# Performance work log

Measured on AMD Instinct MI355X. Metric: run time of the kernel, lower is better.

Reference implementation:

```python
import jax, jax.numpy as jnp
import numpy as np
import math

B, T, TE, D, H = 1, 2048, 1024, 1024, 16
HD = D // H
INF = 1e9  # infinity_proxy from the original module
INIT_SCALE = 0.02


def sinusoid_pos_emb(timesteps, dim):
    # Transformer-XL sinusoids for relative positions [timesteps-1 .. 0].
    inv_freq = 1.0 / (10000.0 ** (np.arange(0, dim, 2) / dim))
    pos_seq = np.arange(timesteps - 1, -1, -1.0)
    inp = np.einsum('i,j->ij', pos_seq, inv_freq)
    return np.concatenate([np.sin(inp), np.cos(inp)], axis=-1).astype(np.float32)


def relative_shift(x):
    # x: [b, h, t, T] -> TXL left-pad / reshape / slice shift trick.
    b, h, t1, t2 = x.shape
    x = jnp.pad(x, ((0, 0), (0, 0), (0, 0), (1, 0)))
    x = x.reshape(b, h, t2 + 1, t1)[:, :, 1:, :]
    return x.reshape(b, h, t1, t2)


def setup_inputs() -> dict:
    key = jax.random.key(0)
    ks = jax.random.split(key, 12)
    s = INIT_SCALE
    x = jax.random.normal(ks[0], (B, T, D), jnp.float32)
    extra = jax.random.normal(ks[1], (B, TE, D), jnp.float32)
    # causal mask over the in-sequence keys; full visibility on the extra memory
    mask = jnp.broadcast_to(jnp.tril(jnp.ones((T, T), jnp.float32))[None, None], (B, 1, T, T))
    extra_mask = jnp.ones((B, 1, T, TE), jnp.float32)
    Wq = jax.random.normal(ks[2], (D, D), jnp.float32) * s
    Wk = jax.random.normal(ks[3], (D, D), jnp.float32) * s
    Wv = jax.random.normal(ks[4], (D, D), jnp.float32) * s
    Wek = jax.random.normal(ks[5], (D, D), jnp.float32) * s
    Wev = jax.random.normal(ks[6], (D, D), jnp.float32) * s
    Wr = jax.random.normal(ks[7], (D, D), jnp.float32) * s
    Wo = jax.random.normal(ks[8], (D, D), jnp.float32) * s
    r_w_bias = jax.random.normal(ks[9], (H, HD), jnp.float32) * s
    r_r_bias = jax.random.normal(ks[10], (H, HD), jnp.float32) * s
    return dict(x=x, extra=extra, mask=mask, extra_mask=extra_mask,
                Wq=Wq, Wk=Wk, Wv=Wv, Wek=Wek, Wev=Wev, Wr=Wr, Wo=Wo,
                r_w_bias=r_w_bias, r_r_bias=r_r_bias)


def reference(x, extra, mask, extra_mask, Wq, Wk, Wv, Wek, Wev, Wr, Wo, r_w_bias, r_r_bias):
    b, t, d = x.shape
    te = extra.shape[1]
    # conv1d(kernel=1, no bias) == matmul projections; cache_steps=0 so y == x
    q = (x @ Wq).reshape(b, t, H, HD)
    k = (x @ Wk).reshape(b, t, H, HD)
    v = (x @ Wv).reshape(b, t, H, HD)
    # Transformer-XL relative-position attend_fn
    pos = jnp.asarray(sinusoid_pos_emb(t, d))            # [t, D]
    r = (pos @ Wr).reshape(t, H, HD)                      # [t, H, HD]
    content = jnp.einsum('bthd,bThd->bhtT', q + r_w_bias, k)
    rel = relative_shift(jnp.einsum('bthd,Thd->bhtT', q + r_r_bias, r))
    attn = content + rel
    attn = attn * mask - INF * (1.0 - mask)
    # extra keys/values use plain dot-product attention (no rel-pos)
    ek = (extra @ Wek).reshape(b, te, H, HD)
    ev = (extra @ Wev).reshape(b, te, H, HD)
    eattn = jnp.einsum('bthd,bThd->bhtT', q, ek)
    eattn = eattn * extra_mask - INF * (1.0 - extra_mask)
    attn = jnp.concatenate([attn, eattn], axis=-1) * (1.0 / math.sqrt(HD))
    p = jax.nn.softmax(attn, axis=-1)
    vv = jnp.concatenate([v, ev], axis=1)                 # [b, t+te, H, HD]
    out = jnp.einsum('bhtT,bThd->bthd', p, vv).reshape(b, t, d)
    return out @ Wo  # final conv1d, with_final_bias=False
```

## Files before the change

### kernel.cpp

```cpp
#include <hip/hip_runtime.h>
#include <hip/hip_bf16.h>
#include <math.h>

#define T_LEN 2048
#define TE_LEN 1024
#define D_DIM 1024
#define H_NUM 16
#define HD_DIM 64
#define R_PAD 64

typedef unsigned short ushort;
typedef __attribute__((ext_vector_type(8))) short short8;
typedef __attribute__((ext_vector_type(4))) float f32x4;
typedef __attribute__((ext_vector_type(4))) ushort ushort4v;

__device__ __forceinline__ ushort f2b(float f) {
    unsigned u = __builtin_bit_cast(unsigned, f);
    u += 0x7fffu + ((u >> 16) & 1u);
    return (ushort)(u >> 16);
}
__device__ __forceinline__ float b2f(ushort s) {
    unsigned u = ((unsigned)s) << 16;
    return __builtin_bit_cast(float, u);
}

__device__ __forceinline__ void gld16(const ushort* g, ushort* l) {
    __builtin_amdgcn_global_load_lds(
        (const __attribute__((address_space(1))) unsigned int*)g,
        (__attribute__((address_space(3))) unsigned int*)l, 16, 0, 0);
}

union U8 { short8 v; ushort u[8]; };

__global__ void prep_kernel(const float* __restrict__ x, const float* __restrict__ extra,
                            ushort* __restrict__ pos, ushort* __restrict__ xb,
                            ushort* __restrict__ eb) {
    const int q = blockIdx.x * 256 + threadIdx.x;
    const int PQ = 524288;
    const int XQ = 1048576;
    if (q < PQ) {
        int idx = q * 4;
        int i = idx >> 10, j = idx & 1023;
        bool sinreg = (j < 512);
        int jj = sinreg ? j : j - 512;
        float p = (float)(2047 - i);
        ushort4v o;
#pragma unroll
        for (int u = 0; u < 4; u++) {
            float inv = exp2f((float)(jj + u) * -0.025952563241f);
            float fa = p * inv;
            ((ushort*)&o)[u] = f2b(sinreg ? sinf(fa) : cosf(fa));
        }
        *(ushort4v*)&pos[idx] = o;
    } else if (q < XQ) {
        int idx = (q - PQ) * 4;
        float4 v = *(const float4*)&x[idx];
        ushort4v o = {f2b(v.x), f2b(v.y), f2b(v.z), f2b(v.w)};
        *(ushort4v*)&xb[idx] = o;
    } else {
        int idx = (q - XQ) * 4;
        float4 v = *(const float4*)&extra[idx];
        ushort4v o = {f2b(v.x), f2b(v.y), f2b(v.z), f2b(v.w)};
        *(ushort4v*)&eb[idx] = o;
    }
}

__global__ __launch_bounds__(256) void transpose7_kernel(
    const float* __restrict__ W0, const float* __restrict__ W1,
    const float* __restrict__ W2, const float* __restrict__ W3,
    const float* __restrict__ W4, const float* __restrict__ W5,
    const float* __restrict__ W6, ushort* __restrict__ out,
    ushort* __restrict__ Rpad) {
    if (blockIdx.z == 7) {
        int gid = (blockIdx.y * 32 + blockIdx.x) * 256 + threadIdx.x;
        if (gid < (R_PAD * 1024) / 8) {
            short8 z = {0, 0, 0, 0, 0, 0, 0, 0};
            *(short8*)&Rpad[gid * 8] = z;
        }
        return;
    }
    const float* Ws[7] = {W0, W1, W2, W3, W4, W5, W6};
    const float* W = Ws[blockIdx.z];
    ushort* WT = out + (size_t)blockIdx.z * (1024 * 1024);
    __shared__ float tile[32][33];
    int c0 = blockIdx.x * 32, r0 = blockIdx.y * 32;
    int tid = threadIdx.x;
#pragma unroll
    for (int p = 0; p < 4; p++) {
        int idx = tid + p * 256;
        int r = idx >> 5, c = idx & 31;
        tile[r][c] = W[(size_t)(r0 + r) * D_DIM + c0 + c];
    }
    __syncthreads();
#pragma unroll
    for (int p = 0; p < 4; p++) {
        int idx = tid + p * 256;
        int r = idx >> 5, c = idx & 31;
        WT[(size_t)(c0 + r) * D_DIM + r0 + c] = f2b(tile[c][r]);
    }
}

__global__ __launch_bounds__(256) void gemm_mega(
    const ushort* __restrict__ xb, const ushort* __restrict__ posb,
    const ushort* __restrict__ eb, const ushort* __restrict__ WT,
    ushort* __restrict__ Qb, ushort* __restrict__ Kb, ushort* __restrict__ VTb,
    ushort* __restrict__ Rb, ushort* __restrict__ EKb, ushort* __restrict__ EVTb) {
    __shared__ ushort As[128 * 64];
    __shared__ ushort Bs[128 * 64];
    const int tid = threadIdx.x;
    const int lane = tid & 63, w = tid >> 6;
    const int l15 = lane & 15, quad = lane >> 4;
    const int wm = w & 1, wn = w >> 1;
    const size_t M1 = 1024 * 1024;

    int idx = blockIdx.x;
    const ushort *A, *BT;
    ushort* dst;
    int m0, nb0, nc0, ldt = 1024;
    bool transp = false;
    if (idx < 384) {
        m0 = (idx & 15) * 128; nb0 = (idx >> 4) * 128;
        A = xb; BT = WT;
        nc0 = nb0 & 1023;
        int seg = nb0 >> 10;
        if (seg == 0) dst = Qb;
        else if (seg == 1) dst = Kb;
        else { dst = VTb; transp = true; ldt = T_LEN; }
    } else if (idx < 512) {
        int i = idx - 384;
        m0 = (i & 15) * 128; nb0 = (i >> 4) * 128; nc0 = nb0;
        A = posb; BT = WT + 5 * M1; dst = Rb;
    } else {
        int i = idx - 512;
        m0 = (i & 7) * 128; nb0 = (i >> 3) * 128; nc0 = nb0 & 1023;
        A = eb; BT = WT + 3 * M1;
        if (nb0 < 1024) dst = EKb;
        else { dst = EVTb; transp = true; ldt = TE_LEN; }
    }

    f32x4 acc[16];
#pragma unroll
    for (int i = 0; i < 16; i++) acc[i] = (f32x4){0.f, 0.f, 0.f, 0.f};

    for (int k0 = 0; k0 < 1024; k0 += 64) {
        __syncthreads();
#pragma unroll
        for (int i = 0; i < 4; i++) {
            int ci = i * 256 + tid;
            int row = ci >> 3, cs = (ci & 7) ^ (row & 7);
            gld16(A + (size_t)(m0 + row) * 1024 + k0 + cs * 8, &As[(i * 32 + w * 8) * 64]);
            gld16(BT + (size_t)(nb0 + row) * 1024 + k0 + cs * 8, &Bs[(i * 32 + w * 8) * 64]);
        }
        __syncthreads();
#pragma unroll
        for (int kc = 0; kc < 2; kc++) {
            short8 bfr[4];
#pragma unroll
            for (int nf = 0; nf < 4; nf++) {
                const int row = wn * 64 + nf * 16 + l15;
                bfr[nf] = *(const short8*)&Bs[(row * 8 + ((kc * 4 + quad) ^ (row & 7))) * 8];
            }
#pragma unroll
            for (int mf = 0; mf < 4; mf++) {
                const int row = wm * 64 + mf * 16 + l15;
                short8 afr = *(const short8*)&As[(row * 8 + ((kc * 4 + quad) ^ (row & 7))) * 8];
#pragma unroll
                for (int nf = 0; nf < 4; nf++)
                    acc[mf * 4 + nf] = __builtin_amdgcn_mfma_f32_16x16x32_bf16(afr, bfr[nf], acc[mf * 4 + nf], 0, 0, 0);
            }
        }
    }

#pragma unroll
    for (int mf = 0; mf < 4; mf++) {
#pragma unroll
        for (int nf = 0; nf < 4; nf++) {
            f32x4 a = acc[mf * 4 + nf];
            const int mrow = m0 + wm * 64 + mf * 16 + quad * 4;
            const int nc = nc0 + wn * 64 + nf * 16 + l15;
            if (transp) {
                ushort4v v = {f2b(a[0]), f2b(a[1]), f2b(a[2]), f2b(a[3])};
                *(ushort4v*)&dst[(size_t)nc * ldt + mrow] = v;
            } else {
#pragma unroll
                for (int r = 0; r < 4; r++) dst[(size_t)(mrow + r) * 1024 + nc] = f2b(a[r]);
            }
        }
    }
}

__global__ __launch_bounds__(256) void gemm_wo(const ushort* __restrict__ A,
                                               const ushort* __restrict__ BT,
                                               float* __restrict__ out) {
    __shared__ ushort As[128 * 64];
    __shared__ ushort Bs[64 * 64];
    const int tid = threadIdx.x;
    const int lane = tid & 63, w = tid >> 6;
    const int l15 = lane & 15, quad = lane >> 4;
    const int wm = w & 1, wn = w >> 1;
    const int m0 = blockIdx.y * 128, n0 = blockIdx.x * 64;

    f32x4 acc[8];
#pragma unroll
    for (int i = 0; i < 8; i++) acc[i] = (f32x4){0.f, 0.f, 0.f, 0.f};

    for (int k0 = 0; k0 < 1024; k0 += 64) {
        __syncthreads();
#pragma unroll
        for (int i = 0; i < 4; i++) {
            int ci = i * 256 + tid;
            int row = ci >> 3, cs = (ci & 7) ^ (row & 7);
            gld16(A + (size_t)(m0 + row) * 1024 + k0 + cs * 8, &As[(i * 32 + w * 8) * 64]);
        }
#pragma unroll
        for (int i = 0; i < 2; i++) {
            int ci = i * 256 + tid;
            int row = ci >> 3, cs = (ci & 7) ^ (row & 7);
            gld16(BT + (size_t)(n0 + row) * 1024 + k0 + cs * 8, &Bs[(i * 32 + w * 8) * 64]);
        }
        __syncthreads();
#pragma unroll
        for (int kc = 0; kc < 2; kc++) {
            short8 bfr[2];
#pragma unroll
            for (int nf = 0; nf < 2; nf++) {
                const int row = wn * 32 + nf * 16 + l15;
                bfr[nf] = *(const short8*)&Bs[(row * 8 + ((kc * 4 + quad) ^ (row & 7))) * 8];
            }
#pragma unroll
            for (int mf = 0; mf < 4; mf++) {
                const int row = wm * 64 + mf * 16 + l15;
                short8 afr = *(const short8*)&As[(row * 8 + ((kc * 4 + quad) ^ (row & 7))) * 8];
#pragma unroll
                for (int nf = 0; nf < 2; nf++)
                    acc[mf * 2 + nf] = __builtin_amdgcn_mfma_f32_16x16x32_bf16(afr, bfr[nf], acc[mf * 2 + nf], 0, 0, 0);
            }
        }
    }

#pragma unroll
    for (int mf = 0; mf < 4; mf++) {
#pragma unroll
        for (int nf = 0; nf < 2; nf++) {
            f32x4 a = acc[mf * 2 + nf];
            const int mrow = m0 + wm * 64 + mf * 16 + quad * 4;
            const int nc = n0 + wn * 32 + nf * 16 + l15;
#pragma unroll
            for (int r = 0; r < 4; r++) out[(size_t)(mrow + r) * 1024 + nc] = a[r];
        }
    }
}

__global__ __launch_bounds__(256) void attn_kernel(
    const ushort* __restrict__ Qb, const ushort* __restrict__ Kb,
    const ushort* __restrict__ VT, const ushort* __restrict__ Rb,
    const ushort* __restrict__ EKb, const ushort* __restrict__ EVT,
    const float* __restrict__ rwb, const float* __restrict__ rrb,
    float* __restrict__ Of, float* __restrict__ lsum) {
    __shared__ ushort Kst[2][32 * 64];
    __shared__ ushort Vst[2][64 * 32];
    __shared__ ushort Rst[128 * 64];
    __shared__ ushort Plds[4][16 * 40];

    const int tid = threadIdx.x;
    const int lane = tid & 63, wl = tid >> 6;
    const int l15 = lane & 15, quad = lane >> 4;
    const int blk = blockIdx.x;
    const int xcd = blk & 7;
    const int u = blk >> 3;
    const int g = u & 1;
    const int v = u >> 1;
    const int rnd = v >> 5, qslot = v & 31;
    const int h = xcd * 2 + rnd;
    const int qt = rnd ? qslot : 31 - qslot;
    const int t0 = qt * 64, tf = t0 + wl * 16;
    const int hbase = h * HD_DIM;
    const int base0 = 1984 - t0;
    const int ninl = qt + 1;
    const int ntotl = ninl + 16;
    const int tt_s = g * ninl;
    const int baseg = base0 + 32 * tt_s;

    short8 qw[2], qr[2], qp[2];
#pragma unroll
    for (int kh = 0; kh < 2; kh++) {
        int dof = hbase + kh * 32 + quad * 8;
        U8 raw; raw.v = *(const short8*)&Qb[(size_t)(tf + l15) * D_DIM + dof];
        U8 a, b, c;
#pragma unroll
        for (int j = 0; j < 8; j++) {
            float f = b2f(raw.u[j]);
            a.u[j] = f2b((f + rwb[dof + j]) * 0.125f);
            b.u[j] = f2b((f + rrb[dof + j]) * 0.125f);
            c.u[j] = f2b(f * 0.125f);
        }
        qw[kh] = a.v; qr[kh] = b.v; qp[kh] = c.v;
    }

    float lr[4] = {0.f, 0.f, 0.f, 0.f};
    f32x4 O[4];
#pragma unroll
    for (int i = 0; i < 4; i++) O[i] = (f32x4){0.f, 0.f, 0.f, 0.f};
    f32x4 rel_carry = (f32x4){0.f, 0.f, 0.f, 0.f};

    auto stageKV = [&](int i2, int buf) {
        const bool ins = i2 < ninl;
        const int j0 = ins ? (tt_s + i2) * 32 : (g * 16 + (i2 - ninl)) * 32;
        const ushort* ksrc = ins ? Kb : EKb;
        const ushort* vsrc = ins ? VT : EVT;
        const int ldv = ins ? T_LEN : TE_LEN;
        {
            int row = tid >> 3, cs = (tid & 7) ^ (row & 7);
            gld16(ksrc + (size_t)(j0 + row) * 1024 + hbase + cs * 8, &Kst[buf][wl * 512]);
        }
        {
            int row = tid >> 2, cs = (tid & 3) ^ (row & 3);
            gld16(vsrc + (size_t)(hbase + row) * ldv + j0 + cs * 8, &Vst[buf][wl * 512]);
        }
    };
    auto stageR = [&](int slotbase, int rowbase) {
        int k = tid >> 3;
        int s = slotbase + k;
        int cs = (tid & 7) ^ (s & 7);
        gld16(Rb + (size_t)(rowbase + k) * 1024 + hbase + cs * 8,
              &Rst[(slotbase + wl * 8) * 64]);
    };

#pragma unroll
    for (int i = 0; i < 3; i++) {
        int ci = i * 256 + tid;
        int k = ci >> 3, cs = (ci & 7) ^ (k & 7);
        gld16(Rb + (size_t)(baseg + k) * 1024 + hbase + cs * 8, &Rst[(i * 32 + wl * 8) * 64]);
    }
    stageKV(0, 0);

    int srcA[4]; bool lowcA[4];
#pragma unroll
    for (int r = 0; r < 4; r++) {
        const int m = quad * 4 + r;
        const int cb = 15 - m + l15;
        srcA[r] = (lane & 48) | (cb & 15);
        lowcA[r] = (cb < 16);
    }

#pragma unroll 1
    for (int i = 0; i < ntotl; i++) {
        const int b = i & 1;
        __syncthreads();
        if (i + 1 < ntotl) {
            stageKV(i + 1, 1 - b);
            if (i + 1 < ninl) stageR((96 + 32 * i) & 127, baseg + 96 + 32 * i);
        }

        const bool ins = i < ninl;
        const int j0 = (tt_s + i) * 32;

        f32x4 con[2];
#pragma unroll
        for (int c = 0; c < 2; c++) con[c] = (f32x4){0.f, 0.f, 0.f, 0.f};
#pragma unroll
        for (int kh = 0; kh < 2; kh++) {
            const short8* qa = ins ? &qw[kh] : &qp[kh];
#pragma unroll
            for (int nh = 0; nh < 2; nh++) {
                const int row = nh * 16 + l15;
                short8 kf = *(const short8*)&Kst[b][(row * 8 + ((kh * 4 + quad) ^ (row & 7))) * 8];
                con[nh] = __builtin_amdgcn_mfma_f32_16x16x32_bf16(*qa, kf, con[nh], 0, 0, 0);
            }
        }

        if (ins) {
            f32x4 relA, rel1, rel2;
            rel1 = (f32x4){0.f, 0.f, 0.f, 0.f};
            rel2 = (f32x4){0.f, 0.f, 0.f, 0.f};
#pragma unroll
            for (int kh = 0; kh < 2; kh++) {
                const int s1 = (64 - 16 * wl + 32 * i + l15) & 127;
                const int s2 = (80 - 16 * wl + 32 * i + l15) & 127;
                short8 rf1 = *(const short8*)&Rst[(s1 * 8 + ((kh * 4 + quad) ^ (s1 & 7))) * 8];
                short8 rf2 = *(const short8*)&Rst[(s2 * 8 + ((kh * 4 + quad) ^ (s2 & 7))) * 8];
                rel1 = __builtin_amdgcn_mfma_f32_16x16x32_bf16(qr[kh], rf1, rel1, 0, 0, 0);
                rel2 = __builtin_amdgcn_mfma_f32_16x16x32_bf16(qr[kh], rf2, rel2, 0, 0, 0);
            }
            if (i == 0) {
                relA = (f32x4){0.f, 0.f, 0.f, 0.f};
#pragma unroll
                for (int kh = 0; kh < 2; kh++) {
                    const int s0 = (48 - 16 * wl + l15) & 127;
                    short8 rf0 = *(const short8*)&Rst[(s0 * 8 + ((kh * 4 + quad) ^ (s0 & 7))) * 8];
                    relA = __builtin_amdgcn_mfma_f32_16x16x32_bf16(qr[kh], rf0, relA, 0, 0, 0);
                }
            } else {
                relA = rel_carry;
            }
            rel_carry = rel2;

            const bool needmask = (j0 + 31 > tf);
#pragma unroll
            for (int r = 0; r < 4; r++) {
                const int m = quad * 4 + r;
                float b0 = __shfl(relA[r], srcA[r]);
                float b1 = __shfl(rel1[r], srcA[r]);
                float b2 = __shfl(rel2[r], srcA[r]);
                float rv0 = lowcA[r] ? b0 : b1, rv1 = lowcA[r] ? b1 : b2;
                float p0 = __expf(con[0][r] + rv0);
                float p1 = __expf(con[1][r] + rv1);
                if (needmask) {
                    const int t = tf + m;
                    if (j0 + l15 > t)      p0 = 0.f;
                    if (j0 + 16 + l15 > t) p1 = 0.f;
                }
                lr[r] += p0 + p1;
                Plds[wl][m * 40 + l15]      = f2b(p0);
                Plds[wl][m * 40 + 16 + l15] = f2b(p1);
            }
        } else {
#pragma unroll
            for (int r = 0; r < 4; r++) {
                const int m = quad * 4 + r;
                float p0 = __expf(con[0][r]);
                float p1 = __expf(con[1][r]);
                lr[r] += p0 + p1;
                Plds[wl][m * 40 + l15]      = f2b(p0);
                Plds[wl][m * 40 + 16 + l15] = f2b(p1);
            }
        }

        short8 pa = *(const short8*)&Plds[wl][l15 * 40 + quad * 8];
#pragma unroll
        for (int df = 0; df < 4; df++) {
            const int row = df * 16 + l15;
            short8 vb = *(const short8*)&Vst[b][(row * 4 + (quad ^ (row & 3))) * 8];
            O[df] = __builtin_amdgcn_mfma_f32_16x16x32_bf16(pa, vb, O[df], 0, 0, 0);
        }
    }

#pragma unroll
    for (int r = 0; r < 4; r++) {
#pragma unroll
        for (int dd = 1; dd < 16; dd <<= 1) lr[r] += __shfl_xor(lr[r], dd);
        const int row = wl * 16 + quad * 4 + r;
        if (l15 == 0) lsum[(size_t)(g * T_LEN + t0 + row) * H_NUM + h] = lr[r];
#pragma unroll
        for (int df = 0; df < 4; df++)
            Of[((size_t)g * T_LEN + t0 + row) * D_DIM + hbase + df * 16 + l15] = O[df][r];
    }
}

__global__ __launch_bounds__(256) void combine_kernel(
    const float* __restrict__ Of, const float* __restrict__ lsum,
    ushort* __restrict__ AOb) {
    const int q = blockIdx.x * 256 + threadIdx.x;
    const int t = q >> 8;
    const int h = (q & 255) >> 4;
    const float inv = 1.0f / (lsum[(size_t)t * H_NUM + h] +
                              lsum[(size_t)(T_LEN + t) * H_NUM + h]);
    float4 a = *(const float4*)&Of[(size_t)q * 4];
    float4 b = *(const float4*)&Of[(size_t)T_LEN * D_DIM + (size_t)q * 4];
    ushort4v o = {f2b((a.x + b.x) * inv), f2b((a.y + b.y) * inv),
                  f2b((a.z + b.z) * inv), f2b((a.w + b.w) * inv)};
    *(ushort4v*)&AOb[(size_t)q * 4] = o;
}

extern "C" void kernel_launch(void* const* d_in, const int* in_sizes, int n_in,
                              void* d_out, int out_size, void* d_ws, size_t ws_size,
                              hipStream_t stream) {
    const float* x     = (const float*)d_in[0];
    const float* extra = (const float*)d_in[1];
    const float* Wq  = (const float*)d_in[4];
    const float* Wk  = (const float*)d_in[5];
    const float* Wv  = (const float*)d_in[6];
    const float* Wek = (const float*)d_in[7];
    const float* Wev = (const float*)d_in[8];
    const float* Wr  = (const float*)d_in[9];
    const float* Wo  = (const float*)d_in[10];
    const float* rwb = (const float*)d_in[11];
    const float* rrb = (const float*)d_in[12];
    float* out = (float*)d_out;

    ushort* ws = (ushort*)d_ws;
    const size_t M1 = 1024 * 1024;
    size_t o = 0;
    ushort* posb = ws + o; o += 2 * M1;
    ushort* xb   = ws + o; o += 2 * M1;
    ushort* eb   = ws + o; o += M1;
    ushort* WT   = ws + o; o += 7 * M1;
    ushort* Qb   = ws + o; o += 2 * M1;
    ushort* Kb   = ws + o; o += 2 * M1;
    ushort* VTb  = ws + o; o += 2 * M1;
    ushort* Rb   = ws + o; o += (size_t)(T_LEN + R_PAD) * 1024;
    ushort* EKb  = ws + o; o += M1;
    ushort* EVTb = ws + o; o += M1;
    ushort* AOb  = posb;
    float* Of    = (float*)(ws + 2 * M1);
    float* lsum  = (float*)(ws + 10 * M1);

    prep_kernel<<<5120, 256, 0, stream>>>(x, extra, posb, xb, eb);
    transpose7_kernel<<<dim3(32, 32, 8), 256, 0, stream>>>(
        Wq, Wk, Wv, Wek, Wev, Wr, Wo, WT, Rb + (size_t)T_LEN * 1024);

    gemm_mega<<<640, 256, 0, stream>>>(xb, posb, eb, WT, Qb, Kb, VTb, Rb, EKb, EVTb);

    attn_kernel<<<1024, 256, 0, stream>>>(Qb, Kb, VTb, Rb, EKb, EVTb, rwb, rrb, Of, lsum);
    combine_kernel<<<2048, 256, 0, stream>>>(Of, lsum, AOb);

    gemm_wo<<<dim3(16, 16), 256, 0, stream>>>(AOb, WT + 6 * M1, out);
}
```

Measured before the change: 264.0 us.

## Shrink relative-position LDS ring buffer to 80 rows and prefetch R fragments

The R ring buffer in shared memory shrinks from 128 to 80 rows, with modulo-80 indexing, to cut LDS use per block and allow more resident blocks. The first relative-score MFMA is hoisted out of the loop, and R fragments for each step are read into registers before the next R tile is staged. The cost is an extra __syncthreads on in-sequence iterations, and the smaller buffer makes the ring-buffer hazards tighter.

After: 260.4 us. Within noise of the previous version (-1.4%).

```diff
diff --git a/kernel.cpp b/kernel.cpp
--- a/kernel.cpp
+++ b/kernel.cpp
@@ -259,7 +259,7 @@
     float* __restrict__ Of, float* __restrict__ lsum) {
     __shared__ ushort Kst[2][32 * 64];
     __shared__ ushort Vst[2][64 * 32];
-    __shared__ ushort Rst[128 * 64];
+    __shared__ ushort Rst[80 * 64];
     __shared__ ushort Plds[4][16 * 40];
 
     const int tid = threadIdx.x;
@@ -301,7 +301,6 @@
     f32x4 O[4];
 #pragma unroll
     for (int i = 0; i < 4; i++) O[i] = (f32x4){0.f, 0.f, 0.f, 0.f};
-    f32x4 rel_carry = (f32x4){0.f, 0.f, 0.f, 0.f};
 
     auto stageKV = [&](int i2, int buf) {
         const bool ins = i2 < ninl;
@@ -318,19 +317,21 @@
             gld16(vsrc + (size_t)(hbase + row) * ldv + j0 + cs * 8, &Vst[buf][wl * 512]);
         }
     };
-    auto stageR = [&](int slotbase, int rowbase) {
+    auto stageR = [&](int sbase, int rowbase) {
         int k = tid >> 3;
-        int s = slotbase + k;
-        int cs = (tid & 7) ^ (s & 7);
-        gld16(Rb + (size_t)(rowbase + k) * 1024 + hbase + cs * 8,
-              &Rst[(slotbase + wl * 8) * 64]);
+        int cs = (tid & 7) ^ (k & 7);
+        int sw = sbase + wl * 8; if (sw >= 80) sw -= 80;
+        gld16(Rb + (size_t)(rowbase + k) * 1024 + hbase + cs * 8, &Rst[sw * 64]);
     };
 
 #pragma unroll
-    for (int i = 0; i < 3; i++) {
-        int ci = i * 256 + tid;
-        int k = ci >> 3, cs = (ci & 7) ^ (k & 7);
-        gld16(Rb + (size_t)(baseg + k) * 1024 + hbase + cs * 8, &Rst[(i * 32 + wl * 8) * 64]);
+    for (int p = 0; p < 3; p++) {
+        int ci = p * 256 + tid;
+        if (ci < 640) {
+            int k = ci >> 3, cs = (ci & 7) ^ (k & 7);
+            gld16(Rb + (size_t)(baseg + k) * 1024 + hbase + cs * 8,
+                  &Rst[(p * 32 + wl * 8) * 64]);
+        }
     }
     stageKV(0, 0);
 
@@ -342,17 +343,59 @@
         srcA[r] = (lane & 48) | (cb & 15);
         lowcA[r] = (cb < 16);
     }
+    int ofs[2];
+#pragma unroll
+    for (int kh = 0; kh < 2; kh++) ofs[kh] = ((kh * 4 + quad) ^ (l15 & 7)) * 8;
+
+    __syncthreads();
+
+    f32x4 rel_carry = (f32x4){0.f, 0.f, 0.f, 0.f};
+    {
+        const int o0 = 48 - 16 * wl + l15;
+#pragma unroll
+        for (int kh = 0; kh < 2; kh++) {
+            short8 rf0 = *(const short8*)&Rst[o0 * 64 + ofs[kh]];
+            rel_carry = __builtin_amdgcn_mfma_f32_16x16x32_bf16(qr[kh], rf0, rel_carry, 0, 0, 0);
+        }
+    }
+    __syncthreads();
+    if (wl < 2) {
+        int k = 80 + (tid >> 3);
+        int cs = (tid & 7) ^ (k & 7);
+        gld16(Rb + (size_t)(baseg + k) * 1024 + hbase + cs * 8, &Rst[(wl * 8) * 64]);
+    }
+
+    int b1 = 64 - 16 * wl + l15;
+    int b2 = b1 + 16; if (b2 >= 80) b2 -= 80;
+    int sbase = 16;
 
 #pragma unroll 1
     for (int i = 0; i < ntotl; i++) {
         const int b = i & 1;
         __syncthreads();
-        if (i + 1 < ntotl) {
+        const bool ins = i < ninl;
+        const bool stR = (i + 1 < ninl);
+
+        short8 rf1[2], rf2[2];
+        if (ins) {
+#pragma unroll
+            for (int kh = 0; kh < 2; kh++) {
+                rf1[kh] = *(const short8*)&Rst[b1 * 64 + ofs[kh]];
+                rf2[kh] = *(const short8*)&Rst[b2 * 64 + ofs[kh]];
+            }
+            b1 += 32; if (b1 >= 80) b1 -= 80;
+            b2 += 32; if (b2 >= 80) b2 -= 80;
+        }
+
+        if (stR) {
+            __syncthreads();
             stageKV(i + 1, 1 - b);
-            if (i + 1 < ninl) stageR((96 + 32 * i) & 127, baseg + 96 + 32 * i);
-        }
-
-        const bool ins = i < ninl;
+            stageR(sbase, baseg + 96 + 32 * i);
+            sbase += 32; if (sbase >= 80) sbase -= 80;
+        } else if (i + 1 < ntotl) {
+            stageKV(i + 1, 1 - b);
+        }
+
         const int j0 = (tt_s + i) * 32;
 
         f32x4 con[2];
@@ -370,28 +413,13 @@
         }
 
         if (ins) {
-            f32x4 relA, rel1, rel2;
-            rel1 = (f32x4){0.f, 0.f, 0.f, 0.f};
-            rel2 = (f32x4){0.f, 0.f, 0.f, 0.f};
+            f32x4 relA = rel_carry;
+            f32x4 rel1 = (f32x4){0.f, 0.f, 0.f, 0.f};
+            f32x4 rel2 = (f32x4){0.f, 0.f, 0.f, 0.f};
 #pragma unroll
             for (int kh = 0; kh < 2; kh++) {
-                const int s1 = (64 - 16 * wl + 32 * i + l15) & 127;
-                const int s2 = (80 - 16 * wl + 32 * i + l15) & 127;
-                short8 rf1 = *(const short8*)&Rst[(s1 * 8 + ((kh * 4 + quad) ^ (s1 & 7))) * 8];
-                short8 rf2 = *(const short8*)&Rst[(s2 * 8 + ((kh * 4 + quad) ^ (s2 & 7))) * 8];
-                rel1 = __builtin_amdgcn_mfma_f32_16x16x32_bf16(qr[kh], rf1, rel1, 0, 0, 0);
-                rel2 = __builtin_amdgcn_mfma_f32_16x16x32_bf16(qr[kh], rf2, rel2, 0, 0, 0);
-            }
-            if (i == 0) {
-                relA = (f32x4){0.f, 0.f, 0.f, 0.f};
-#pragma unroll
-                for (int kh = 0; kh < 2; kh++) {
-                    const int s0 = (48 - 16 * wl + l15) & 127;
-                    short8 rf0 = *(const short8*)&Rst[(s0 * 8 + ((kh * 4 + quad) ^ (s0 & 7))) * 8];
-                    relA = __builtin_amdgcn_mfma_f32_16x16x32_bf16(qr[kh], rf0, relA, 0, 0, 0);
-                }
-            } else {
-                relA = rel_carry;
+                rel1 = __builtin_amdgcn_mfma_f32_16x16x32_bf16(qr[kh], rf1[kh], rel1, 0, 0, 0);
+                rel2 = __builtin_amdgcn_mfma_f32_16x16x32_bf16(qr[kh], rf2[kh], rel2, 0, 0, 0);
             }
             rel_carry = rel2;
 
@@ -400,9 +428,9 @@
             for (int r = 0; r < 4; r++) {
                 const int m = quad * 4 + r;
                 float b0 = __shfl(relA[r], srcA[r]);
-                float b1 = __shfl(rel1[r], srcA[r]);
-                float b2 = __shfl(rel2[r], srcA[r]);
-                float rv0 = lowcA[r] ? b0 : b1, rv1 = lowcA[r] ? b1 : b2;
+                float b1v = __shfl(rel1[r], srcA[r]);
+                float b2v = __shfl(rel2[r], srcA[r]);
+                float rv0 = lowcA[r] ? b0 : b1v, rv1 = lowcA[r] ? b1v : b2v;
                 float p0 = __expf(con[0][r] + rv0);
                 float p1 = __expf(con[1][r] + rv1);
                 if (needmask) {
```
